# Optimization experiments

Hardware: AMD Instinct MI355X
Metric: run time of the kernel (lower is better)

The kernel has to match this reference:

```python
import jax, jax.numpy as jnp
import numpy as np

B, L, H, P = 16, 4096, 512, 256
LN_EPS = 1e-6  # flax nnx.LayerNorm default


def setup_inputs() -> dict:
    key = jax.random.key(0)
    ks = jax.random.split(key, 9)
    dt_min, dt_max = 1e-3, 1e-1
    x = jax.random.normal(ks[0], (B, L, H), dtype=jnp.float32)
    # lecun-normal-like scaling for B (fan_in = H) and C (fan_in = P)
    return {
        "x": x,
        "log_lambda_re": jax.random.normal(ks[1], (P,), dtype=jnp.float32),
        "lambda_im": jax.random.normal(ks[2], (P,), dtype=jnp.float32) * 3.0,
        "B_re": jax.random.normal(ks[3], (P, H), dtype=jnp.float32) / np.sqrt(H),
        "B_im": jax.random.normal(ks[4], (P, H), dtype=jnp.float32) / np.sqrt(H),
        "C_re": jax.random.normal(ks[5], (H, P), dtype=jnp.float32) / np.sqrt(P),
        "C_im": jax.random.normal(ks[6], (H, P), dtype=jnp.float32) / np.sqrt(P),
        "D": jax.random.normal(ks[7], (H,), dtype=jnp.float32),
        "log_step": jax.random.uniform(ks[8], (P,), dtype=jnp.float32)
        * (np.log(dt_max) - np.log(dt_min)) + np.log(dt_min),
        "ln_scale": jnp.ones((H,), dtype=jnp.float32),
        "ln_bias": jnp.zeros((H,), dtype=jnp.float32),
    }


def _binary_operator(q_i, q_j):
    A_i, b_i = q_i
    A_j, b_j = q_j
    return (A_j * A_i, A_j * b_i + b_j)


def reference(x, log_lambda_re, lambda_im, B_re, B_im, C_re, C_im, D, log_step,
              ln_scale, ln_bias):
    Lambda = -jnp.exp(log_lambda_re) + 1j * lambda_im          # [P] complex
    B_tilde = B_re + 1j * B_im                                  # [P,H]
    C_tilde = C_re + 1j * C_im                                  # [H,P]
    step = jnp.exp(log_step)                                    # [P]
    # ZOH discretization
    Lambda_bar = jnp.exp(Lambda * step)                         # [P]
    B_bar = ((Lambda_bar - 1.0) / Lambda)[:, None] * B_tilde    # [P,H]
    # SSM via parallel associative scan over the length axis
    Bu = x @ B_bar.T                                            # [B,L,P] complex
    Lambda_el = jnp.broadcast_to(Lambda_bar, Bu.shape)          # [B,L,P]
    _, xs = jax.lax.associative_scan(_binary_operator, (Lambda_el, Bu), axis=-2)
    ys = 2.0 * (xs @ C_tilde.T).real                            # [B,L,H]
    y = ys + x * D
    y = jax.nn.gelu(y)
    # residual + LayerNorm
    z = x + y
    mean = jnp.mean(z, axis=-1, keepdims=True)
    var = jnp.var(z, axis=-1, keepdims=True)
    return (z - mean) * jax.lax.rsqrt(var + LN_EPS) * ln_scale + ln_bias
```

## Files before the change

kernel.cpp:

```cpp
#include <hip/hip_runtime.h>
#include <hip/hip_bf16.h>
#include <cstdint>
#include <cstddef>

typedef short bf16x8 __attribute__((ext_vector_type(8)));
typedef float f32x4  __attribute__((ext_vector_type(4)));

#define HH 512
#define PP 256
#define LL 4096
#define BBATCH 16
#define MM (BBATCH * LL)
#define NCHUNK 128
#define SCHUNK 32
#define NGRP 16
#define GCH 8

__device__ __forceinline__ unsigned short f2bf(float f) {
  union { float f; unsigned u; } v; v.f = f;
  unsigned r = (v.u + 0x7FFFu + ((v.u >> 16) & 1u)) >> 16;
  return (unsigned short)r;
}
__device__ __forceinline__ float bf2f(unsigned short b) {
  return __uint_as_float(((unsigned)b) << 16);
}

__device__ __forceinline__ void async16(const void* g, void* l) {
  __builtin_amdgcn_global_load_lds(
      (const __attribute__((address_space(1))) unsigned*)g,
      (__attribute__((address_space(3))) unsigned*)l, 16, 0, 0);
}

__global__ void precompute_params(const float* __restrict__ llr_,
                                  const float* __restrict__ lim_,
                                  const float* __restrict__ lstep_,
                                  float* __restrict__ lam) {
  int p = threadIdx.x;
  if (p >= PP) return;
  float Lr = -expf(llr_[p]);
  float Li = lim_[p];
  float st = expf(lstep_[p]);
  float mag = expf(Lr * st);
  float ang = Li * st;
  float lbr = mag * cosf(ang);
  float lbi = mag * sinf(ang);
  float den = Lr * Lr + Li * Li;
  float nr = lbr - 1.f, ni = lbi;
  float cr = (nr * Lr + ni * Li) / den;
  float ci = (ni * Lr - nr * Li) / den;
  float m32 = expf(32.f * Lr * st);
  float a32r = m32 * cosf(32.f * ang);
  float a32i = m32 * sinf(32.f * ang);
  float m256 = expf(256.f * Lr * st);
  float a256r = m256 * cosf(256.f * ang);
  float a256i = m256 * sinf(256.f * ang);
  lam[p]            = lbr;
  lam[PP + p]       = lbi;
  lam[2 * PP + p]   = a32r;
  lam[3 * PP + p]   = a32i;
  lam[4 * PP + p]   = cr;
  lam[5 * PP + p]   = ci;
  lam[6 * PP + p]   = a256r;
  lam[7 * PP + p]   = a256i;
}

__global__ void build_weights(const float* __restrict__ B_re,
                              const float* __restrict__ B_im,
                              const float* __restrict__ C_re,
                              const float* __restrict__ C_im,
                              const float* __restrict__ lam,
                              unsigned short* __restrict__ Bcat,
                              unsigned short* __restrict__ Ccat) {
  int bid = blockIdx.x;
  int tid = threadIdx.x;
  if (bid < 512) {
    int n = bid;
    int p = n >> 1;
    int is_re = !(n & 1);
    float cr = lam[4 * PP + p], ci = lam[5 * PP + p];
    for (int c = tid; c < HH; c += 256) {
      float br = B_re[(size_t)p * HH + c];
      float bi = B_im[(size_t)p * HH + c];
      float v = is_re ? (cr * br - ci * bi) : (cr * bi + ci * br);
      Bcat[(size_t)n * HH + c] = f2bf(v);
    }
  } else {
    int h = bid - 512;
    for (int c = tid; c < HH; c += 256) {
      int p = c >> 1;
      float v = !(c & 1) ? 2.f * C_re[(size_t)h * PP + p]
                         : -2.f * C_im[(size_t)h * PP + p];
      Ccat[(size_t)h * HH + c] = f2bf(v);
    }
  }
}

__global__ __launch_bounds__(256) void cvt_x_bf16(const float* __restrict__ x,
                                                  unsigned short* __restrict__ xb) {
  const float4* x4 = (const float4*)x;
  ushort4* o4 = (ushort4*)xb;
  int stride = 2048 * 256;
  for (int i = blockIdx.x * 256 + threadIdx.x; i < (MM * HH / 4); i += stride) {
    float4 v = x4[i];
    ushort4 o;
    o.x = f2bf(v.x); o.y = f2bf(v.y); o.z = f2bf(v.z); o.w = f2bf(v.w);
    o4[i] = o;
  }
}

template <int EPI>
__global__ __launch_bounds__(256) void gemm_bt(const unsigned short* __restrict__ A,
                                               const unsigned short* __restrict__ Bt,
                                               const unsigned short* xf,
                                               const float* __restrict__ Dv,
                                               unsigned short* Cout) {
  __shared__ __align__(16) unsigned short As[2][8192];
  __shared__ __align__(16) unsigned short Bs[2][8192];
  const int tid = threadIdx.x, lane = tid & 63, w = tid >> 6;
  const int bid = blockIdx.x;
  const int logical = (bid & 7) * 64 + (bid >> 3);
  const int nt = logical & 3, mg = logical >> 2;
  const int n0 = nt * 128;
  const int r = lane & 15, g = lane >> 4;
  const int wm = (w >> 1) * 64, wn = (w & 1) * 64;
  const int swz = (r & 7) << 4;

  int sW[4], srow[4], scol[4];
#pragma unroll
  for (int j = 0; j < 4; ++j) {
    int idx = w * 4 + j;
    int W = idx * 1024 + lane * 16;
    sW[j] = W;
    srow[j] = W >> 7;
    scol[j] = (W & 127) ^ (((W >> 7) & 7) << 4);
  }
  const char* Ab = (const char*)A;
  const char* Bb = (const char*)Bt;
  char* As0 = (char*)&As[0][0];
  char* Bs0 = (char*)&Bs[0][0];

  f32x4 acc[4][4];
#pragma unroll
  for (int a2 = 0; a2 < 4; ++a2)
#pragma unroll
    for (int b2 = 0; b2 < 4; ++b2) acc[a2][b2] = (f32x4){0.f, 0.f, 0.f, 0.f};

#define STAGE_(buf_, s_) { \
    int m0_ = (mg * 4 + ((s_) >> 3)) * 128; \
    int kb_ = ((s_) & 7) * 128; \
    char* dA_ = As0 + (buf_) * 16384; \
    char* dB_ = Bs0 + (buf_) * 16384; \
    _Pragma("unroll") \
    for (int j = 0; j < 4; ++j) { \
      async16(Ab + (size_t)(m0_ + srow[j]) * 1024 + kb_ + scol[j], dA_ + sW[j]); \
      async16(Bb + (size_t)(n0  + srow[j]) * 1024 + kb_ + scol[j], dB_ + sW[j]); \
    } }

  STAGE_(0, 0);
  asm volatile("s_waitcnt vmcnt(0)" ::: "memory");
  __syncthreads();

  int cur = 0;
  for (int s = 0; s < 32; ++s) {
    if (s < 31) STAGE_(cur ^ 1, s + 1);
    const char* rdA = As0 + cur * 16384;
    const char* rdB = Bs0 + cur * 16384;
#pragma unroll
    for (int kk = 0; kk < 2; ++kk) {
      bf16x8 af[4], bv[4];
#pragma unroll
      for (int mi = 0; mi < 4; ++mi)
        af[mi] = *(const bf16x8*)(rdA + (wm + mi * 16 + r) * 128 +
                                  ((kk * 64 + g * 16) ^ swz));
#pragma unroll
      for (int ni = 0; ni < 4; ++ni)
        bv[ni] = *(const bf16x8*)(rdB + (wn + ni * 16 + r) * 128 +
                                  ((kk * 64 + g * 16) ^ swz));
#pragma unroll
      for (int mi = 0; mi < 4; ++mi)
#pragma unroll
        for (int ni = 0; ni < 4; ++ni)
          acc[mi][ni] = __builtin_amdgcn_mfma_f32_16x16x32_bf16(
              af[mi], bv[ni], acc[mi][ni], 0, 0, 0);
    }
    if ((s & 7) == 7) {
      int m0 = (mg * 4 + (s >> 3)) * 128;
#pragma unroll
      for (int mi = 0; mi < 4; ++mi)
#pragma unroll
        for (int ni = 0; ni < 4; ++ni) {
          int col = n0 + wn + ni * 16 + r;
          float Dh = (EPI == 1) ? Dv[col] : 0.f;
#pragma unroll
          for (int j = 0; j < 4; ++j) {
            int row = m0 + wm + mi * 16 + g * 4 + j;
            float v = acc[mi][ni][j];
            if (EPI == 0) {
              Cout[(size_t)row * 512 + col] = f2bf(v);
            } else {
              float xv = bf2f(xf[(size_t)row * 512 + col]);
              float t = v + xv * Dh;
              float u2 = 0.7978845608028654f * (t + 0.044715f * t * t * t);
              float e = __expf(2.f * u2);
              float th = 1.f - 2.f / (e + 1.f);
              float y = 0.5f * t * (1.f + th);
              Cout[(size_t)row * 512 + col] = f2bf(xv + y);
            }
            acc[mi][ni][j] = 0.f;
          }
        }
    }
    asm volatile("s_waitcnt vmcnt(0)" ::: "memory");
    __syncthreads();
    cur ^= 1;
  }
#undef STAGE_
}

__global__ __launch_bounds__(256) void scan_carry(const unsigned short* __restrict__ Bu,
                                                  const float* __restrict__ lam,
                                                  float* __restrict__ carry) {
  int bid = blockIdx.x;
  int b = bid >> 7, c = bid & 127;
  int p = threadIdx.x;
  float ar = lam[p], ai = lam[PP + p];
  float sr = 0.f, si = 0.f;
  size_t base = ((size_t)b * LL + (size_t)c * SCHUNK) * 512;
#pragma unroll
  for (int i = 0; i < SCHUNK; ++i) {
    unsigned u = ((const unsigned*)(Bu + base + (size_t)i * 512))[p];
    float ur = bf2f((unsigned short)(u & 0xFFFFu));
    float ui = bf2f((unsigned short)(u >> 16));
    float nr = ar * sr - ai * si + ur;
    float ni = ar * si + ai * sr + ui;
    sr = nr; si = ni;
  }
  ((float2*)(carry + (size_t)bid * 512))[p] = make_float2(sr, si);
}

__global__ void chain_a(const float* __restrict__ carry,
                        const float* __restrict__ lam,
                        float* __restrict__ gcarry) {
  int bid = blockIdx.x;
  int b = bid >> 4, g2 = bid & 15;
  int p = threadIdx.x;
  float ar = lam[2 * PP + p], ai = lam[3 * PP + p];
  float sr = 0.f, si = 0.f;
#pragma unroll
  for (int i = 0; i < GCH; ++i) {
    int c = g2 * GCH + i;
    float2 cv = ((const float2*)(carry + (size_t)(b * NCHUNK + c) * 512))[p];
    float nr = cv.x + ar * sr - ai * si;
    float ni = cv.y + ar * si + ai * sr;
    sr = nr; si = ni;
  }
  ((float2*)(gcarry + (size_t)bid * 512))[p] = make_float2(sr, si);
}

__global__ void chain_b(const float* __restrict__ gcarry,
                        const float* __restrict__ lam,
                        float* __restrict__ gstate) {
  int b = blockIdx.x;
  int p = threadIdx.x;
  float ar = lam[6 * PP + p], ai = lam[7 * PP + p];
  float sr = 0.f, si = 0.f;
#pragma unroll
  for (int g2 = 0; g2 < NGRP; ++g2) {
    float2 cv = ((const float2*)(gcarry + (size_t)(b * NGRP + g2) * 512))[p];
    ((float2*)(gstate + (size_t)(b * NGRP + g2) * 512))[p] = make_float2(sr, si);
    float nr = cv.x + ar * sr - ai * si;
    float ni = cv.y + ar * si + ai * sr;
    sr = nr; si = ni;
  }
}

__global__ void chain_c(float* carry,
                        const float* __restrict__ lam,
                        const float* __restrict__ gstate) {
  int bid = blockIdx.x;
  int b = bid >> 4, g2 = bid & 15;
  int p = threadIdx.x;
  float ar = lam[2 * PP + p], ai = lam[3 * PP + p];
  float2 s0 = ((const float2*)(gstate + (size_t)bid * 512))[p];
  float sr = s0.x, si = s0.y;
#pragma unroll
  for (int i = 0; i < GCH; ++i) {
    int c = g2 * GCH + i;
    float2* slot = ((float2*)(carry + (size_t)(b * NCHUNK + c) * 512)) + p;
    float2 cv = *slot;
    *slot = make_float2(sr, si);
    float nr = cv.x + ar * sr - ai * si;
    float ni = cv.y + ar * si + ai * sr;
    sr = nr; si = ni;
  }
}

__global__ __launch_bounds__(256) void scan_final(unsigned short* Bu,
                                                  const float* __restrict__ lam,
                                                  const float* __restrict__ carry) {
  int bid = blockIdx.x;
  int b = bid >> 7, c = bid & 127;
  int p = threadIdx.x;
  float ar = lam[p], ai = lam[PP + p];
  float2 s0 = ((const float2*)(carry + (size_t)bid * 512))[p];
  float sr = s0.x, si = s0.y;
  size_t base = ((size_t)b * LL + (size_t)c * SCHUNK) * 512;
#pragma unroll
  for (int i = 0; i < SCHUNK; ++i) {
    unsigned* slot = ((unsigned*)(Bu + base + (size_t)i * 512)) + p;
    unsigned u = *slot;
    float ur = bf2f((unsigned short)(u & 0xFFFFu));
    float ui = bf2f((unsigned short)(u >> 16));
    float nr = ar * sr - ai * si + ur;
    float ni = ar * si + ai * sr + ui;
    sr = nr; si = ni;
    *slot = (unsigned)f2bf(sr) | ((unsigned)f2bf(si) << 16);
  }
}

__global__ __launch_bounds__(256) void ln_kernel(const unsigned short* __restrict__ z,
                                                 const float* __restrict__ scale,
                                                 const float* __restrict__ bias,
                                                 float* __restrict__ out) {
  int tid = threadIdx.x, lane = tid & 63, wv = tid >> 6;
  int gw = blockIdx.x * 4 + wv;
  int c0 = lane * 8;
  float sc[8], bi[8];
#pragma unroll
  for (int j = 0; j < 8; ++j) { sc[j] = scale[c0 + j]; bi[j] = bias[c0 + j]; }
  for (int row = gw; row < MM; row += 8192) {
    uint4 zv = *(const uint4*)(z + (size_t)row * 512 + c0);
    float f[8];
    f[0] = __uint_as_float(zv.x << 16); f[1] = __uint_as_float(zv.x & 0xFFFF0000u);
    f[2] = __uint_as_float(zv.y << 16); f[3] = __uint_as_float(zv.y & 0xFFFF0000u);
    f[4] = __uint_as_float(zv.z << 16); f[5] = __uint_as_float(zv.z & 0xFFFF0000u);
    f[6] = __uint_as_float(zv.w << 16); f[7] = __uint_as_float(zv.w & 0xFFFF0000u);
    float s = 0.f, s2 = 0.f;
#pragma unroll
    for (int j = 0; j < 8; ++j) { s += f[j]; s2 += f[j] * f[j]; }
#pragma unroll
    for (int o = 32; o; o >>= 1) {
      s += __shfl_xor(s, o, 64);
      s2 += __shfl_xor(s2, o, 64);
    }
    float mean = s * (1.f / 512.f);
    float var = s2 * (1.f / 512.f) - mean * mean;
    float inv = rsqrtf(var + 1e-6f);
    float o8[8];
#pragma unroll
    for (int j = 0; j < 8; ++j) o8[j] = (f[j] - mean) * inv * sc[j] + bi[j];
    float4* op = (float4*)(out + (size_t)row * 512 + c0);
    op[0] = make_float4(o8[0], o8[1], o8[2], o8[3]);
    op[1] = make_float4(o8[4], o8[5], o8[6], o8[7]);
  }
}

extern "C" void kernel_launch(void* const* d_in, const int* in_sizes, int n_in,
                              void* d_out, int out_size, void* d_ws, size_t ws_size,
                              hipStream_t stream) {
  const float* x    = (const float*)d_in[0];
  const float* llr  = (const float*)d_in[1];
  const float* lim  = (const float*)d_in[2];
  const float* B_re = (const float*)d_in[3];
  const float* B_im = (const float*)d_in[4];
  const float* C_re = (const float*)d_in[5];
  const float* C_im = (const float*)d_in[6];
  const float* Dv   = (const float*)d_in[7];
  const float* lstep= (const float*)d_in[8];
  const float* lnsc = (const float*)d_in[9];
  const float* lnbi = (const float*)d_in[10];
  float* out = (float*)d_out;

  char* ws = (char*)d_ws;
  unsigned short* xb   = (unsigned short*)(ws);
  unsigned short* bu   = (unsigned short*)(ws + 67108864);
  unsigned short* bcat = (unsigned short*)(ws + 134217728);
  unsigned short* ccat = (unsigned short*)(ws + 134742016);
  float* lam           = (float*)(ws + 135266304);
  float* carry         = (float*)(ws + 135274496);
  float* gcarry        = (float*)(ws + 139468800);
  float* gstate        = (float*)(ws + 139993088);

  precompute_params<<<1, 256, 0, stream>>>(llr, lim, lstep, lam);
  build_weights<<<1024, 256, 0, stream>>>(B_re, B_im, C_re, C_im, lam, bcat, ccat);
  cvt_x_bf16<<<2048, 256, 0, stream>>>(x, xb);
  gemm_bt<0><<<512, 256, 0, stream>>>(xb, bcat, nullptr, nullptr, bu);
  scan_carry<<<2048, 256, 0, stream>>>(bu, lam, carry);
  chain_a<<<256, 256, 0, stream>>>(carry, lam, gcarry);
  chain_b<<<16, 256, 0, stream>>>(gcarry, lam, gstate);
  chain_c<<<256, 256, 0, stream>>>(carry, lam, gstate);
  scan_final<<<2048, 256, 0, stream>>>(bu, lam, carry);
  gemm_bt<1><<<512, 256, 0, stream>>>(bu, ccat, xb, Dv, xb);
  ln_kernel<<<2048, 256, 0, stream>>>(xb, lnsc, lnbi, out);
}
```

Measured before the change: 472.8 us.

## Move GELU epilogue into LayerNorm, fuse chunk chain kernels, pipeline GEMM loads

The GELU/residual epilogue moves out of the second GEMM into the LayerNorm kernel, which now reads fp32 x directly and applies D, GELU and the residual before normalising. The three-kernel hierarchical carry chain becomes one sequential 128-step kernel with 16 blocks. The GEMM main loop is restructured with precomputed advancing pointers, partial vmcnt waits, raw s_barriers and setprio around the MFMA block to overlap loads with compute. The single chain kernel has very low parallelism and a long serial dependency, and LN now reads fp32 x, which adds memory traffic.

```diff
diff --git a/kernel.cpp b/kernel.cpp
--- a/kernel.cpp
+++ b/kernel.cpp
@@ -13,8 +13,6 @@
 #define MM (BBATCH * LL)
 #define NCHUNK 128
 #define SCHUNK 32
-#define NGRP 16
-#define GCH 8
 
 __device__ __forceinline__ unsigned short f2bf(float f) {
   union { float f; unsigned u; } v; v.f = f;
@@ -51,17 +49,12 @@
   float m32 = expf(32.f * Lr * st);
   float a32r = m32 * cosf(32.f * ang);
   float a32i = m32 * sinf(32.f * ang);
-  float m256 = expf(256.f * Lr * st);
-  float a256r = m256 * cosf(256.f * ang);
-  float a256i = m256 * sinf(256.f * ang);
   lam[p]            = lbr;
   lam[PP + p]       = lbi;
   lam[2 * PP + p]   = a32r;
   lam[3 * PP + p]   = a32i;
   lam[4 * PP + p]   = cr;
   lam[5 * PP + p]   = ci;
-  lam[6 * PP + p]   = a256r;
-  lam[7 * PP + p]   = a256i;
 }
 
 __global__ void build_weights(const float* __restrict__ B_re,
@@ -108,12 +101,9 @@
   }
 }
 
-template <int EPI>
 __global__ __launch_bounds__(256) void gemm_bt(const unsigned short* __restrict__ A,
                                                const unsigned short* __restrict__ Bt,
-                                               const unsigned short* xf,
-                                               const float* __restrict__ Dv,
-                                               unsigned short* Cout) {
+                                               unsigned short* __restrict__ Cout) {
   __shared__ __align__(16) unsigned short As[2][8192];
   __shared__ __align__(16) unsigned short Bs[2][8192];
   const int tid = threadIdx.x, lane = tid & 63, w = tid >> 6;
@@ -125,17 +115,23 @@
   const int wm = (w >> 1) * 64, wn = (w & 1) * 64;
   const int swz = (r & 7) << 4;
 
-  int sW[4], srow[4], scol[4];
-#pragma unroll
-  for (int j = 0; j < 4; ++j) {
-    int idx = w * 4 + j;
-    int W = idx * 1024 + lane * 16;
-    sW[j] = W;
-    srow[j] = W >> 7;
-    scol[j] = (W & 127) ^ (((W >> 7) & 7) << 4);
-  }
-  const char* Ab = (const char*)A;
-  const char* Bb = (const char*)Bt;
+  int sW[4];
+  const char* pA[4];
+  const char* pB[4];
+  {
+    const char* Ab = (const char*)A;
+    const char* Bb = (const char*)Bt;
+#pragma unroll
+    for (int j = 0; j < 4; ++j) {
+      int idx = w * 4 + j;
+      int W = idx * 1024 + lane * 16;
+      sW[j] = W;
+      int row = W >> 7;
+      int colb = (W & 127) ^ ((row & 7) << 4);
+      pA[j] = Ab + (size_t)(mg * 512 + row) * 1024 + colb;
+      pB[j] = Bb + (size_t)(n0 + row) * 1024 + colb;
+    }
+  }
   char* As0 = (char*)&As[0][0];
   char* Bs0 = (char*)&Bs[0][0];
 
@@ -145,26 +141,38 @@
 #pragma unroll
     for (int b2 = 0; b2 < 4; ++b2) acc[a2][b2] = (f32x4){0.f, 0.f, 0.f, 0.f};
 
-#define STAGE_(buf_, s_) { \
-    int m0_ = (mg * 4 + ((s_) >> 3)) * 128; \
-    int kb_ = ((s_) & 7) * 128; \
+#define STAGE_(buf_) { \
     char* dA_ = As0 + (buf_) * 16384; \
     char* dB_ = Bs0 + (buf_) * 16384; \
     _Pragma("unroll") \
     for (int j = 0; j < 4; ++j) { \
-      async16(Ab + (size_t)(m0_ + srow[j]) * 1024 + kb_ + scol[j], dA_ + sW[j]); \
-      async16(Bb + (size_t)(n0  + srow[j]) * 1024 + kb_ + scol[j], dB_ + sW[j]); \
+      async16(pA[j], dA_ + sW[j]); \
+      async16(pB[j], dB_ + sW[j]); \
     } }
-
-  STAGE_(0, 0);
-  asm volatile("s_waitcnt vmcnt(0)" ::: "memory");
-  __syncthreads();
-
-  int cur = 0;
+#define ADV_(dest_) { \
+    int dAi_ = (((dest_) & 7) == 0) ? 130176 : 128; \
+    int dBi_ = (((dest_) & 7) == 0) ? -896 : 128; \
+    _Pragma("unroll") \
+    for (int j = 0; j < 4; ++j) { pA[j] += dAi_; pB[j] += dBi_; } }
+
+  STAGE_(0);
+  ADV_(1);
+
   for (int s = 0; s < 32; ++s) {
-    if (s < 31) STAGE_(cur ^ 1, s + 1);
-    const char* rdA = As0 + cur * 16384;
-    const char* rdB = Bs0 + cur * 16384;
+    if (s < 31) {
+      STAGE_((s + 1) & 1);
+      ADV_(s + 2);
+      asm volatile("s_waitcnt vmcnt(8)" ::: "memory");
+    } else {
+      asm volatile("s_waitcnt vmcnt(0)" ::: "memory");
+    }
+    __builtin_amdgcn_sched_barrier(0);
+    __builtin_amdgcn_s_barrier();
+    __builtin_amdgcn_sched_barrier(0);
+
+    const char* rdA = As0 + (s & 1) * 16384;
+    const char* rdB = Bs0 + (s & 1) * 16384;
+    __builtin_amdgcn_s_setprio(1);
 #pragma unroll
     for (int kk = 0; kk < 2; ++kk) {
       bf16x8 af[4], bv[4];
@@ -183,6 +191,11 @@
           acc[mi][ni] = __builtin_amdgcn_mfma_f32_16x16x32_bf16(
               af[mi], bv[ni], acc[mi][ni], 0, 0, 0);
     }
+    __builtin_amdgcn_s_setprio(0);
+    __builtin_amdgcn_sched_barrier(0);
+    __builtin_amdgcn_s_barrier();
+    __builtin_amdgcn_sched_barrier(0);
+
     if ((s & 7) == 7) {
       int m0 = (mg * 4 + (s >> 3)) * 128;
 #pragma unroll
@@ -190,31 +203,17 @@
 #pragma unroll
         for (int ni = 0; ni < 4; ++ni) {
           int col = n0 + wn + ni * 16 + r;
-          float Dh = (EPI == 1) ? Dv[col] : 0.f;
 #pragma unroll
           for (int j = 0; j < 4; ++j) {
             int row = m0 + wm + mi * 16 + g * 4 + j;
-            float v = acc[mi][ni][j];
-            if (EPI == 0) {
-              Cout[(size_t)row * 512 + col] = f2bf(v);
-            } else {
-              float xv = bf2f(xf[(size_t)row * 512 + col]);
-              float t = v + xv * Dh;
-              float u2 = 0.7978845608028654f * (t + 0.044715f * t * t * t);
-              float e = __expf(2.f * u2);
-              float th = 1.f - 2.f / (e + 1.f);
-              float y = 0.5f * t * (1.f + th);
-              Cout[(size_t)row * 512 + col] = f2bf(xv + y);
-            }
+            Cout[(size_t)row * 512 + col] = f2bf(acc[mi][ni][j]);
             acc[mi][ni][j] = 0.f;
           }
         }
     }
-    asm volatile("s_waitcnt vmcnt(0)" ::: "memory");
-    __syncthreads();
-    cur ^= 1;
   }
 #undef STAGE_
+#undef ADV_
 }
 
 __global__ __launch_bounds__(256) void scan_carry(const unsigned short* __restrict__ Bu,
@@ -238,57 +237,16 @@
   ((float2*)(carry + (size_t)bid * 512))[p] = make_float2(sr, si);
 }
 
-__global__ void chain_a(const float* __restrict__ carry,
-                        const float* __restrict__ lam,
-                        float* __restrict__ gcarry) {
-  int bid = blockIdx.x;
-  int b = bid >> 4, g2 = bid & 15;
+__global__ void chain_fused(float* carry, const float* __restrict__ lam) {
+  int b = blockIdx.x;
   int p = threadIdx.x;
   float ar = lam[2 * PP + p], ai = lam[3 * PP + p];
   float sr = 0.f, si = 0.f;
-#pragma unroll
-  for (int i = 0; i < GCH; ++i) {
-    int c = g2 * GCH + i;
-    float2 cv = ((const float2*)(carry + (size_t)(b * NCHUNK + c) * 512))[p];
-    float nr = cv.x + ar * sr - ai * si;
-    float ni = cv.y + ar * si + ai * sr;
-    sr = nr; si = ni;
-  }
-  ((float2*)(gcarry + (size_t)bid * 512))[p] = make_float2(sr, si);
-}
-
-__global__ void chain_b(const float* __restrict__ gcarry,
-                        const float* __restrict__ lam,
-                        float* __restrict__ gstate) {
-  int b = blockIdx.x;
-  int p = threadIdx.x;
-  float ar = lam[6 * PP + p], ai = lam[7 * PP + p];
-  float sr = 0.f, si = 0.f;
-#pragma unroll
-  for (int g2 = 0; g2 < NGRP; ++g2) {
-    float2 cv = ((const float2*)(gcarry + (size_t)(b * NGRP + g2) * 512))[p];
-    ((float2*)(gstate + (size_t)(b * NGRP + g2) * 512))[p] = make_float2(sr, si);
-    float nr = cv.x + ar * sr - ai * si;
-    float ni = cv.y + ar * si + ai * sr;
-    sr = nr; si = ni;
-  }
-}
-
-__global__ void chain_c(float* carry,
-                        const float* __restrict__ lam,
-                        const float* __restrict__ gstate) {
-  int bid = blockIdx.x;
-  int b = bid >> 4, g2 = bid & 15;
-  int p = threadIdx.x;
-  float ar = lam[2 * PP + p], ai = lam[3 * PP + p];
-  float2 s0 = ((const float2*)(gstate + (size_t)bid * 512))[p];
-  float sr = s0.x, si = s0.y;
-#pragma unroll
-  for (int i = 0; i < GCH; ++i) {
-    int c = g2 * GCH + i;
-    float2* slot = ((float2*)(carry + (size_t)(b * NCHUNK + c) * 512)) + p;
-    float2 cv = *slot;
-    *slot = make_float2(sr, si);
+  float2* c2 = ((float2*)carry) + (size_t)b * NCHUNK * 256 + p;
+#pragma unroll 8
+  for (int c = 0; c < NCHUNK; ++c) {
+    float2 cv = c2[(size_t)c * 256];
+    c2[(size_t)c * 256] = make_float2(sr, si);
     float nr = cv.x + ar * sr - ai * si;
     float ni = cv.y + ar * si + ai * sr;
     sr = nr; si = ni;
@@ -318,26 +276,43 @@
   }
 }
 
-__global__ __launch_bounds__(256) void ln_kernel(const unsigned short* __restrict__ z,
-                                                 const float* __restrict__ scale,
-                                                 const float* __restrict__ bias,
-                                                 float* __restrict__ out) {
+__global__ __launch_bounds__(256) void ln_fused(const unsigned short* __restrict__ ys,
+                                                const float* __restrict__ x,
+                                                const float* __restrict__ Dv,
+                                                const float* __restrict__ scale,
+                                                const float* __restrict__ bias,
+                                                float* __restrict__ out) {
   int tid = threadIdx.x, lane = tid & 63, wv = tid >> 6;
   int gw = blockIdx.x * 4 + wv;
   int c0 = lane * 8;
-  float sc[8], bi[8];
-#pragma unroll
-  for (int j = 0; j < 8; ++j) { sc[j] = scale[c0 + j]; bi[j] = bias[c0 + j]; }
+  float sc[8], bi[8], Dh[8];
+#pragma unroll
+  for (int j = 0; j < 8; ++j) {
+    sc[j] = scale[c0 + j]; bi[j] = bias[c0 + j]; Dh[j] = Dv[c0 + j];
+  }
   for (int row = gw; row < MM; row += 8192) {
-    uint4 zv = *(const uint4*)(z + (size_t)row * 512 + c0);
-    float f[8];
-    f[0] = __uint_as_float(zv.x << 16); f[1] = __uint_as_float(zv.x & 0xFFFF0000u);
-    f[2] = __uint_as_float(zv.y << 16); f[3] = __uint_as_float(zv.y & 0xFFFF0000u);
-    f[4] = __uint_as_float(zv.z << 16); f[5] = __uint_as_float(zv.z & 0xFFFF0000u);
-    f[6] = __uint_as_float(zv.w << 16); f[7] = __uint_as_float(zv.w & 0xFFFF0000u);
+    uint4 yv = *(const uint4*)(ys + (size_t)row * 512 + c0);
+    float yf[8];
+    yf[0] = bf2f((unsigned short)(yv.x & 0xFFFFu)); yf[1] = bf2f((unsigned short)(yv.x >> 16));
+    yf[2] = bf2f((unsigned short)(yv.y & 0xFFFFu)); yf[3] = bf2f((unsigned short)(yv.y >> 16));
+    yf[4] = bf2f((unsigned short)(yv.z & 0xFFFFu)); yf[5] = bf2f((unsigned short)(yv.z >> 16));
+    yf[6] = bf2f((unsigned short)(yv.w & 0xFFFFu)); yf[7] = bf2f((unsigned short)(yv.w >> 16));
+    const float4* xp = (const float4*)(x + (size_t)row * 512 + c0);
+    float4 xv0 = xp[0], xv1 = xp[1];
+    float xf[8] = {xv0.x, xv0.y, xv0.z, xv0.w, xv1.x, xv1.y, xv1.z, xv1.w};
+    float zf[8];
     float s = 0.f, s2 = 0.f;
 #pragma unroll
-    for (int j = 0; j < 8; ++j) { s += f[j]; s2 += f[j] * f[j]; }
+    for (int j = 0; j < 8; ++j) {
+      float t = yf[j] + xf[j] * Dh[j];
+      float u2 = 0.7978845608028654f * (t + 0.044715f * t * t * t);
+      float e = __expf(2.f * u2);
+      float th = 1.f - 2.f / (e + 1.f);
+      float y = 0.5f * t * (1.f + th);
+      float z = xf[j] + y;
+      zf[j] = z;
+      s += z; s2 += z * z;
+    }
 #pragma unroll
     for (int o = 32; o; o >>= 1) {
       s += __shfl_xor(s, o, 64);
@@ -348,7 +323,7 @@
     float inv = rsqrtf(var + 1e-6f);
     float o8[8];
 #pragma unroll
-    for (int j = 0; j < 8; ++j) o8[j] = (f[j] - mean) * inv * sc[j] + bi[j];
+    for (int j = 0; j < 8; ++j) o8[j] = (zf[j] - mean) * inv * sc[j] + bi[j];
     float4* op = (float4*)(out + (size_t)row * 512 + c0);
     op[0] = make_float4(o8[0], o8[1], o8[2], o8[3]);
     op[1] = make_float4(o8[4], o8[5], o8[6], o8[7]);
@@ -378,18 +353,14 @@
   unsigned short* ccat = (unsigned short*)(ws + 134742016);
   float* lam           = (float*)(ws + 135266304);
   float* carry         = (float*)(ws + 135274496);
-  float* gcarry        = (float*)(ws + 139468800);
-  float* gstate        = (float*)(ws + 139993088);
 
   precompute_params<<<1, 256, 0, stream>>>(llr, lim, lstep, lam);
   build_weights<<<1024, 256, 0, stream>>>(B_re, B_im, C_re, C_im, lam, bcat, ccat);
   cvt_x_bf16<<<2048, 256, 0, stream>>>(x, xb);
-  gemm_bt<0><<<512, 256, 0, stream>>>(xb, bcat, nullptr, nullptr, bu);
+  gemm_bt<<<512, 256, 0, stream>>>(xb, bcat, bu);
   scan_carry<<<2048, 256, 0, stream>>>(bu, lam, carry);
-  chain_a<<<256, 256, 0, stream>>>(carry, lam, gcarry);
-  chain_b<<<16, 256, 0, stream>>>(gcarry, lam, gstate);
-  chain_c<<<256, 256, 0, stream>>>(carry, lam, gstate);
+  chain_fused<<<16, 256, 0, stream>>>(carry, lam);
   scan_final<<<2048, 256, 0, stream>>>(bu, lam, carry);
-  gemm_bt<1><<<512, 256, 0, stream>>>(bu, ccat, xb, Dv, xb);
-  ln_kernel<<<2048, 256, 0, stream>>>(xb, lnsc, lnbi, out);
-}
+  gemm_bt<<<512, 256, 0, stream>>>(bu, ccat, xb);
+  ln_fused<<<2048, 256, 0, stream>>>(xb, x, Dv, lnsc, lnbi, out);
+}
```

After: 435.7 us. 7.9% less time.
